# Optimization experiments

Hardware: AMD Instinct MI355X
Metric: run time of the kernel (lower is better)

The kernel has to match this reference:

```python
import jax, jax.numpy as jnp
import numpy as np

IN_CH, HID, OUT = 128, 128, 47

def _sage_conv(x_src, x_dst, src, dst, n_dst, Wl, bl, Wr):
    # mean aggregation of source features onto destination nodes
    msg_sum = jax.ops.segment_sum(x_src[src], dst, num_segments=n_dst)
    deg = jax.ops.segment_sum(jnp.ones((src.shape[0],), x_src.dtype), dst, num_segments=n_dst)
    agg = msg_sum / jnp.maximum(deg, 1.0)[:, None]
    return agg @ Wl + bl + x_dst @ Wr


def setup_inputs() -> dict:
    key = jax.random.key(0)
    ks = jax.random.split(key, 12)
    N0, N1, N2 = 200000, 100000, 20000
    E0, E1 = 1600000, 320000
    def glorot(k, fan_in, fan_out):
        s = jnp.sqrt(6.0 / (fan_in + fan_out))
        return jax.random.uniform(k, (fan_in, fan_out), jnp.float32, -s, s)
    return {
        'x': jax.random.normal(ks[0], (N0, IN_CH), jnp.float32),
        'src0': jax.random.randint(ks[1], (E0,), 0, N0),
        'dst0': jax.random.randint(ks[2], (E0,), 0, N1),
        'src1': jax.random.randint(ks[3], (E1,), 0, N1),
        'dst1': jax.random.randint(ks[4], (E1,), 0, N2),
        'n1': N1,
        'n2': N2,
        'Wl0': glorot(ks[5], IN_CH, HID),
        'bl0': jnp.zeros((HID,), jnp.float32),
        'Wr0': glorot(ks[6], IN_CH, HID),
        'Wl1': glorot(ks[7], HID, OUT),
        'bl1': jnp.zeros((OUT,), jnp.float32),
        'Wr1': glorot(ks[8], HID, OUT),
    }


def reference(x, src0, dst0, src1, dst1, n1, n2, Wl0, bl0, Wr0, Wl1, bl1, Wr1):
    # layer 0: bipartite SAGEConv + relu (dropout is identity in eval mode)
    h = _sage_conv(x, x[:n1], src0, dst0, n1, Wl0, bl0, Wr0)
    h = jax.nn.relu(h)
    # layer 1: SAGEConv to output classes
    out = _sage_conv(h, h[:n2], src1, dst1, n2, Wl1, bl1, Wr1)
    return jax.nn.log_softmax(out, axis=-1)
```

## Files before the change

### kernel.cpp

```cpp
#include <hip/hip_runtime.h>
#include <hip/hip_bf16.h>
#include <math.h>

#define N1_ROWS 100000
#define N2_ROWS 20000
#define CH 128
#define OUTC 47
#define CAP 6144
#define SCHUNK 4096

typedef __attribute__((ext_vector_type(8))) short short8;
typedef __attribute__((ext_vector_type(4))) float floatx4;

__device__ inline ushort f2b(float f) {
    union { __hip_bfloat16 b; ushort u; } cv;
    cv.b = __float2bfloat16(f);
    return cv.u;
}
__device__ inline float b2f_lo(uint u) { return __uint_as_float(u << 16); }
__device__ inline float b2f_hi(uint u) { return __uint_as_float(u & 0xffff0000u); }

__device__ inline void scatter_body(
    const int* __restrict__ src, const int* __restrict__ dst,
    uint* __restrict__ gcur, uint* __restrict__ ebuf, int E, int NB,
    int sb, uint* hist, uint* runb)
{
    const int base = sb * SCHUNK;
    const int t = threadIdx.x;

    uint d[16], s[16];
    bool ok[4];
    #pragma unroll
    for (int j = 0; j < 4; ++j) {
        int e = base + j * 1024 + t * 4;
        ok[j] = (e < E);
        if (ok[j]) {
            uint4 dv = *(const uint4*)(dst + e);
            uint4 sv = *(const uint4*)(src + e);
            d[j*4+0] = dv.x; d[j*4+1] = dv.y; d[j*4+2] = dv.z; d[j*4+3] = dv.w;
            s[j*4+0] = sv.x; s[j*4+1] = sv.y; s[j*4+2] = sv.z; s[j*4+3] = sv.w;
        }
    }

    for (int b = t; b < 512; b += 256) hist[b] = 0;
    __syncthreads();
    #pragma unroll
    for (int j = 0; j < 4; ++j)
        if (ok[j]) {
            #pragma unroll
            for (int k = 0; k < 4; ++k) atomicAdd(&hist[d[j*4+k] >> 8], 1u);
        }
    __syncthreads();
    for (int b = t; b < NB; b += 256) {
        uint c = hist[b];
        runb[b] = c ? atomicAdd(&gcur[b], c) : 0u;
        hist[b] = 0;
    }
    __syncthreads();
    #pragma unroll
    for (int j = 0; j < 4; ++j)
        if (ok[j]) {
            #pragma unroll
            for (int k = 0; k < 4; ++k) {
                uint dd = d[j*4+k];
                uint b = dd >> 8;
                uint off = runb[b] + atomicAdd(&hist[b], 1u);
                if (off < CAP)
                    ebuf[(size_t)b * CAP + off] = ((dd & 255u) << 18) | s[j*4+k];
            }
        }
}

__global__ __launch_bounds__(256) void prep(
    const float* __restrict__ x, ushort* __restrict__ xb, int n4,
    const int* __restrict__ src0, const int* __restrict__ dst0,
    uint* __restrict__ gcur0, uint* __restrict__ ebuf0, int E0, int NB0,
    const int* __restrict__ src1, const int* __restrict__ dst1,
    uint* __restrict__ gcur1, uint* __restrict__ ebuf1, int E1, int NB1,
    const float* __restrict__ Wl0, const float* __restrict__ Wr0,
    const float* __restrict__ Wl1, const float* __restrict__ Wr1,
    const float* __restrict__ bl1,
    ushort* __restrict__ W0p, ushort* __restrict__ W1p, float* __restrict__ bl1p,
    int CB, int S0, int S1)
{
    __shared__ uint hist[512];
    __shared__ uint runb[512];
    int blk = blockIdx.x;
    if (blk < S0) {
        scatter_body(src0, dst0, gcur0, ebuf0, E0, NB0, blk, hist, runb);
    } else if (blk < S0 + S1) {
        scatter_body(src1, dst1, gcur1, ebuf1, E1, NB1, blk - S0, hist, runb);
    } else if (blk == S0 + S1) {
        int t = threadIdx.x;
        for (int c = t; c < 4096; c += 256) {
            int n = c & 127; int kb = (c >> 7) & 15; int p = c >> 11;
            const float* W = p ? Wr0 : Wl0;
            __align__(16) ushort tmp[8];
            #pragma unroll
            for (int i = 0; i < 8; ++i) tmp[i] = f2b(W[(kb * 8 + i) * CH + n]);
            *(uint4*)(W0p + (size_t)c * 8) = *(const uint4*)tmp;
        }
    } else if (blk == S0 + S1 + 1) {
        int t = threadIdx.x;
        for (int c = t; c < 1536; c += 256) {
            int n = c % 48; int kb = (c / 48) & 15; int p = c / 768;
            const float* W = p ? Wr1 : Wl1;
            __align__(16) ushort tmp[8];
            #pragma unroll
            for (int i = 0; i < 8; ++i)
                tmp[i] = (n < OUTC) ? f2b(W[(kb * 8 + i) * OUTC + n]) : (ushort)0;
            *(uint4*)(W1p + (size_t)c * 8) = *(const uint4*)tmp;
        }
        if (t < 48) bl1p[t] = (t < OUTC) ? bl1[t] : -3.0e38f;
    } else {
        int i = (blk - S0 - S1 - 2) * 256 + threadIdx.x;
        if (i < n4) {
            float4 v = ((const float4*)x)[i];
            ushort4 o;
            o.x = f2b(v.x); o.y = f2b(v.y); o.z = f2b(v.z); o.w = f2b(v.w);
            ((ushort4*)xb)[i] = o;
        }
    }
}

__global__ __launch_bounds__(256) void csr_all(
    const uint* __restrict__ ebuf0, const uint* __restrict__ gcur0,
    int* __restrict__ idx0, int* __restrict__ deg0, int* __restrict__ rs0,
    int NB0, int n1,
    const uint* __restrict__ ebuf1, const uint* __restrict__ gcur1,
    int* __restrict__ idx1, int* __restrict__ deg1, int* __restrict__ rs1,
    int NB1, int n2)
{
    int b = blockIdx.x;
    const uint* ebuf; const uint* gcur;
    int* idx; int* deg; int* rs; int n;
    if (b < NB0) { ebuf = ebuf0; gcur = gcur0; idx = idx0; deg = deg0; rs = rs0; n = n1; }
    else { b -= NB0; ebuf = ebuf1; gcur = gcur1; idx = idx1; deg = deg1; rs = rs1; n = n2; }

    int t = threadIdx.x;
    __shared__ uint gsh[512];
    __shared__ uint psc[256];
    __shared__ uint hist[256];
    __shared__ uint sc[256];
    __shared__ uint lrs[256];
    __shared__ uint idxl[CAP];

    uint c0 = gcur[2 * t];     if (c0 > CAP) c0 = CAP;
    uint c1 = gcur[2 * t + 1]; if (c1 > CAP) c1 = CAP;
    uint pv = c0 + c1;
    psc[t] = pv;
    __syncthreads();
    for (int off = 1; off < 256; off <<= 1) {
        uint val = (t >= off) ? psc[t - off] : 0;
        __syncthreads();
        psc[t] += val;
        __syncthreads();
    }
    uint epair = psc[t] - pv;
    gsh[2 * t] = epair;
    gsh[2 * t + 1] = epair + c0;
    __syncthreads();

    uint cnt = gcur[b]; if (cnt > CAP) cnt = CAP;
    uint bout = gsh[b];
    size_t bin = (size_t)b * CAP;
    int row0 = b << 8;
    int nrows = n - row0; if (nrows > 256) nrows = 256;

    hist[t] = 0;
    __syncthreads();
    for (uint i0 = 0; i0 < cnt; i0 += 1024) {
        uint i = i0 + t * 4;
        uint v0 = 0, v1 = 0, v2 = 0, v3 = 0; int nv = 0;
        if (i + 3 < cnt) {
            uint4 vv = *(const uint4*)(ebuf + bin + i);
            v0 = vv.x; v1 = vv.y; v2 = vv.z; v3 = vv.w; nv = 4;
        } else if (i < cnt) {
            nv = (int)(cnt - i);
            v0 = ebuf[bin + i];
            if (nv > 1) v1 = ebuf[bin + i + 1];
            if (nv > 2) v2 = ebuf[bin + i + 2];
        }
        if (nv > 0) atomicAdd(&hist[v0 >> 18], 1u);
        if (nv > 1) atomicAdd(&hist[v1 >> 18], 1u);
        if (nv > 2) atomicAdd(&hist[v2 >> 18], 1u);
        if (nv > 3) atomicAdd(&hist[v3 >> 18], 1u);
    }
    __syncthreads();
    uint hv = hist[t];
    sc[t] = hv;
    __syncthreads();
    for (int off = 1; off < 256; off <<= 1) {
        uint val = (t >= off) ? sc[t - off] : 0;
        __syncthreads();
        sc[t] += val;
        __syncthreads();
    }
    uint lbase = sc[t] - hv;
    if (t < nrows) { deg[row0 + t] = (int)hv; rs[row0 + t] = (int)(bout + lbase); }
    lrs[t] = lbase;
    hist[t] = 0;
    __syncthreads();
    for (uint i0 = 0; i0 < cnt; i0 += 1024) {
        uint i = i0 + t * 4;
        uint v0 = 0, v1 = 0, v2 = 0, v3 = 0; int nv = 0;
        if (i + 3 < cnt) {
            uint4 vv = *(const uint4*)(ebuf + bin + i);
            v0 = vv.x; v1 = vv.y; v2 = vv.z; v3 = vv.w; nv = 4;
        } else if (i < cnt) {
            nv = (int)(cnt - i);
            v0 = ebuf[bin + i];
            if (nv > 1) v1 = ebuf[bin + i + 1];
            if (nv > 2) v2 = ebuf[bin + i + 2];
        }
        if (nv > 0) { uint r = v0 >> 18; idxl[lrs[r] + atomicAdd(&hist[r], 1u)] = v0 & 0x3FFFFu; }
        if (nv > 1) { uint r = v1 >> 18; idxl[lrs[r] + atomicAdd(&hist[r], 1u)] = v1 & 0x3FFFFu; }
        if (nv > 2) { uint r = v2 >> 18; idxl[lrs[r] + atomicAdd(&hist[r], 1u)] = v2 & 0x3FFFFu; }
        if (nv > 3) { uint r = v3 >> 18; idxl[lrs[r] + atomicAdd(&hist[r], 1u)] = v3 & 0x3FFFFu; }
    }
    __syncthreads();
    for (uint i = t; i < cnt; i += 256) idx[bout + i] = (int)idxl[i];
}

__global__ __launch_bounds__(256) void gather_mean_bb(
    const ushort* __restrict__ xb,
    const int* __restrict__ idx,
    const int* __restrict__ rs,
    const int* __restrict__ deg,
    ushort* __restrict__ aggb,
    int n)
{
    int row = blockIdx.x * 4 + (threadIdx.x >> 6);
    int lane = threadIdx.x & 63;
    if (row >= n) return;
    int start = rs[row];
    int cnt = deg[row];
    const uint* x2 = (const uint*)xb;
    float ax = 0.0f, ay = 0.0f;
    int i = 0;
    for (; i + 3 < cnt; i += 4) {
        int s0 = idx[start + i];
        int s1 = idx[start + i + 1];
        int s2 = idx[start + i + 2];
        int s3 = idx[start + i + 3];
        uint v0 = x2[(size_t)s0 * 64 + lane];
        uint v1 = x2[(size_t)s1 * 64 + lane];
        uint v2 = x2[(size_t)s2 * 64 + lane];
        uint v3 = x2[(size_t)s3 * 64 + lane];
        ax += (b2f_lo(v0) + b2f_lo(v1)) + (b2f_lo(v2) + b2f_lo(v3));
        ay += (b2f_hi(v0) + b2f_hi(v1)) + (b2f_hi(v2) + b2f_hi(v3));
    }
    for (; i < cnt; ++i) {
        uint v0 = x2[(size_t)idx[start + i] * 64 + lane];
        ax += b2f_lo(v0);
        ay += b2f_hi(v0);
    }
    float inv = 1.0f / fmaxf((float)cnt, 1.0f);
    uint o = (uint)f2b(ax * inv) | ((uint)f2b(ay * inv) << 16);
    ((uint*)aggb)[(size_t)row * 64 + lane] = o;
}

#define TM 128
__global__ __launch_bounds__(256) void gemm_mfma(
    const ushort* __restrict__ Apan,
    const ushort* __restrict__ Bpan,
    const ushort* __restrict__ Wp,
    const float* __restrict__ bias,
    ushort* __restrict__ H,
    int rows)
{
    __shared__ __align__(16) ushort As[16384];
    __shared__ __align__(16) ushort Ws[16384];

    const int tid = threadIdx.x;
    const int lane = tid & 63;
    const int wave = tid >> 6;
    const int q = lane >> 4;
    const int ln = lane & 15;
    const int rbase = blockIdx.x * TM;
    const int mrow = wave * 32;

    floatx4 acc[2][8];
    #pragma unroll
    for (int i = 0; i < 2; ++i)
        #pragma unroll
        for (int j = 0; j < 8; ++j)
            acc[i][j] = (floatx4)0.0f;

    #pragma unroll 1
    for (int phase = 0; phase < 2; ++phase) {
        const ushort* Ag = phase ? Bpan : Apan;

        {
            int m0 = tid & 15;
            int c  = tid >> 4;
            #pragma unroll
            for (int j = 0; j < 8; ++j) {
                int m = m0 + 16 * j;
                uint4 v = *(const uint4*)(Ag + (size_t)(rbase + m) * CH + c * 8);
                *(uint4*)(As + ((size_t)c * 128 + m) * 8) = v;
            }
        }
        {
            const uint4* Wg4 = (const uint4*)(Wp + phase * 16384);
            uint4* Ws4 = (uint4*)Ws;
            for (int i = tid; i < 2048; i += 256) Ws4[i] = Wg4[i];
        }
        __syncthreads();

        #pragma unroll
        for (int k = 0; k < 4; ++k) {
            int kb = k * 4 + q;
            short8 b[8];
            #pragma unroll
            for (int nt = 0; nt < 8; ++nt)
                b[nt] = *(const short8*)(Ws + ((size_t)kb * 128 + nt * 16 + ln) * 8);
            #pragma unroll
            for (int mt = 0; mt < 2; ++mt) {
                short8 a = *(const short8*)(As + ((size_t)kb * 128 + mrow + mt * 16 + ln) * 8);
                #pragma unroll
                for (int nt = 0; nt < 8; ++nt)
                    acc[mt][nt] = __builtin_amdgcn_mfma_f32_16x16x32_bf16(
                        a, b[nt], acc[mt][nt], 0, 0, 0);
            }
        }
        __syncthreads();
    }

    float bj[8];
    #pragma unroll
    for (int nt = 0; nt < 8; ++nt) bj[nt] = bias[nt * 16 + ln];

    #pragma unroll
    for (int mt = 0; mt < 2; ++mt) {
        #pragma unroll
        for (int r = 0; r < 4; ++r) {
            int grow = rbase + mrow + mt * 16 + q * 4 + r;
            if (grow < rows) {
                #pragma unroll
                for (int nt = 0; nt < 8; ++nt) {
                    float v = acc[mt][nt][r] + bj[nt];
                    v = fmaxf(v, 0.0f);
                    H[(size_t)grow * CH + nt * 16 + ln] = f2b(v);
                }
            }
        }
    }
}

__global__ __launch_bounds__(256) void gemm_mfma_l1(
    const ushort* __restrict__ Apan,
    const ushort* __restrict__ Bpan,
    const ushort* __restrict__ Wp,
    const float* __restrict__ biasp,
    float* __restrict__ out,
    int rows)
{
    __shared__ __align__(16) ushort As[16384];
    __shared__ __align__(16) ushort Ws[6144];

    const int tid = threadIdx.x;
    const int lane = tid & 63;
    const int wave = tid >> 6;
    const int q = lane >> 4;
    const int ln = lane & 15;
    const int rbase = blockIdx.x * TM;
    const int mrow = wave * 32;

    floatx4 acc[2][3];
    #pragma unroll
    for (int i = 0; i < 2; ++i)
        #pragma unroll
        for (int j = 0; j < 3; ++j)
            acc[i][j] = (floatx4)0.0f;

    #pragma unroll 1
    for (int phase = 0; phase < 2; ++phase) {
        const ushort* Ag = phase ? Bpan : Apan;
        {
            int m0 = tid & 15;
            int c  = tid >> 4;
            #pragma unroll
            for (int j = 0; j < 8; ++j) {
                int m = m0 + 16 * j;
                uint4 v = *(const uint4*)(Ag + (size_t)(rbase + m) * CH + c * 8);
                *(uint4*)(As + ((size_t)c * 128 + m) * 8) = v;
            }
        }
        {
            const uint4* Wg4 = (const uint4*)(Wp + phase * 6144);
            uint4* Ws4 = (uint4*)Ws;
            for (int i = tid; i < 768; i += 256) Ws4[i] = Wg4[i];
        }
        __syncthreads();

        #pragma unroll
        for (int k = 0; k < 4; ++k) {
            int kb = k * 4 + q;
            short8 b0 = *(const short8*)(Ws + ((size_t)kb * 48 +  0 + ln) * 8);
            short8 b1 = *(const short8*)(Ws + ((size_t)kb * 48 + 16 + ln) * 8);
            short8 b2 = *(const short8*)(Ws + ((size_t)kb * 48 + 32 + ln) * 8);
            #pragma unroll
            for (int mt = 0; mt < 2; ++mt) {
                short8 a = *(const short8*)(As + ((size_t)kb * 128 + mrow + mt * 16 + ln) * 8);
                acc[mt][0] = __builtin_amdgcn_mfma_f32_16x16x32_bf16(a, b0, acc[mt][0], 0, 0, 0);
                acc[mt][1] = __builtin_amdgcn_mfma_f32_16x16x32_bf16(a, b1, acc[mt][1], 0, 0, 0);
                acc[mt][2] = __builtin_amdgcn_mfma_f32_16x16x32_bf16(a, b2, acc[mt][2], 0, 0, 0);
            }
        }
        __syncthreads();
    }

    float b0 = biasp[ln], b1 = biasp[16 + ln], b2 = biasp[32 + ln];

    #pragma unroll
    for (int mt = 0; mt < 2; ++mt) {
        #pragma unroll
        for (int r = 0; r < 4; ++r) {
            int grow = rbase + mrow + mt * 16 + q * 4 + r;
            float v0 = acc[mt][0][r] + b0;
            float v1 = acc[mt][1][r] + b1;
            float v2 = acc[mt][2][r] + b2;
            float mx = fmaxf(v0, fmaxf(v1, v2));
            #pragma unroll
            for (int off = 1; off < 16; off <<= 1) mx = fmaxf(mx, __shfl_xor(mx, off));
            float s = expf(v0 - mx) + expf(v1 - mx) + expf(v2 - mx);
            #pragma unroll
            for (int off = 1; off < 16; off <<= 1) s += __shfl_xor(s, off);
            float ls = mx + logf(s);
            if (grow < rows) {
                out[(size_t)grow * OUTC + ln] = v0 - ls;
                out[(size_t)grow * OUTC + 16 + ln] = v1 - ls;
                if (32 + ln < OUTC) out[(size_t)grow * OUTC + 32 + ln] = v2 - ls;
            }
        }
    }
}

extern "C" void kernel_launch(void* const* d_in, const int* in_sizes, int n_in,
                              void* d_out, int out_size, void* d_ws, size_t ws_size,
                              hipStream_t stream) {
    const float* x    = (const float*)d_in[0];
    const int*   src0 = (const int*)d_in[1];
    const int*   dst0 = (const int*)d_in[2];
    const int*   src1 = (const int*)d_in[3];
    const int*   dst1 = (const int*)d_in[4];
    const float* Wl0  = (const float*)d_in[7];
    const float* bl0  = (const float*)d_in[8];
    const float* Wr0  = (const float*)d_in[9];
    const float* Wl1  = (const float*)d_in[10];
    const float* bl1  = (const float*)d_in[11];
    const float* Wr1  = (const float*)d_in[12];
    float* out = (float*)d_out;

    const int E0 = in_sizes[1];
    const int E1 = in_sizes[3];
    const int n0 = in_sizes[0] / CH;
    const int n1 = N1_ROWS, n2 = N2_ROWS;
    const int n1pad = ((n1 + TM - 1) / TM) * TM;
    const int n2pad = ((n2 + TM - 1) / TM) * TM;
    const int NB0 = (n1 + 255) >> 8;
    const int NB1 = (n2 + 255) >> 8;

    ushort* xb   = (ushort*)d_ws;
    ushort* aggb = xb + (size_t)n0 * CH;
    ushort* h    = aggb + (size_t)n1pad * CH;
    ushort* W0p  = h + (size_t)n1 * CH;
    ushort* W1p  = W0p + 32768;
    float*  bl1p = (float*)(W1p + 12288);
    int*    idx0 = (int*)(bl1p + 48);
    int*    deg0 = idx0 + E0;
    int*    rs0  = deg0 + n1;
    int*    idx1 = rs0 + n1;
    int*    deg1 = idx1 + E1;
    int*    rs1  = deg1 + n2;
    uint*   gcur0 = (uint*)(rs1 + n2);
    uint*   gcur1 = gcur0 + 512;

    uint* ebuf0 = (uint*)aggb;
    uint* ebuf1 = (uint*)h;
    ushort* agg1b = aggb;

    const int n4 = n0 * CH / 4;
    const int CB = (n4 + 255) / 256;
    const int S0 = (E0 + SCHUNK - 1) / SCHUNK;
    const int S1 = (E1 + SCHUNK - 1) / SCHUNK;

    hipMemsetAsync(gcur0, 0, 1024 * sizeof(uint), stream);
    prep<<<S0 + S1 + 2 + CB, 256, 0, stream>>>(
        x, xb, n4,
        src0, dst0, gcur0, ebuf0, E0, NB0,
        src1, dst1, gcur1, ebuf1, E1, NB1,
        Wl0, Wr0, Wl1, Wr1, bl1, W0p, W1p, bl1p,
        CB, S0, S1);
    csr_all<<<NB0 + NB1, 256, 0, stream>>>(
        ebuf0, gcur0, idx0, deg0, rs0, NB0, n1,
        ebuf1, gcur1, idx1, deg1, rs1, NB1, n2);
    gather_mean_bb<<<(n1 + 3) / 4, 256, 0, stream>>>(xb, idx0, rs0, deg0, aggb, n1);
    gemm_mfma<<<n1pad / TM, 256, 0, stream>>>(aggb, xb, W0p, bl0, h, n1);
    gather_mean_bb<<<(n2 + 3) / 4, 256, 0, stream>>>(h, idx1, rs1, deg1, agg1b, n2);
    gemm_mfma_l1<<<n2pad / TM, 256, 0, stream>>>(agg1b, h, W1p, bl1p, out, n2);
}
```

Measured before the change: 328.4 us.

## Fuse layer-0 CSR build with mean gather in one 1024-thread kernel

For layer 0, the CSR bucket sort now keeps the sorted source indices in shared memory, and the same block immediately gathers and averages the bf16 features for its 256 destination rows. This removes the global idx0/deg0/rs0 writes and reads and one kernel launch. Blocks grow to 1024 threads, and the layer-1 block offset is computed with a 512-wide scan over gcur1 only. Edge buckets move into the h buffer so aggb can be written during the fused kernel. In exchange, each block has 16 waves gathering rows and a large shared-memory footprint, which may reduce occupancy.

```diff
diff --git a/kernel.cpp b/kernel.cpp
--- a/kernel.cpp
+++ b/kernel.cpp
@@ -123,103 +123,184 @@
     }
 }
 
-__global__ __launch_bounds__(256) void csr_all(
+__global__ __launch_bounds__(1024) void csr_gather(
     const uint* __restrict__ ebuf0, const uint* __restrict__ gcur0,
-    int* __restrict__ idx0, int* __restrict__ deg0, int* __restrict__ rs0,
-    int NB0, int n1,
+    const ushort* __restrict__ xb, ushort* __restrict__ aggb, int NB0, int n1,
     const uint* __restrict__ ebuf1, const uint* __restrict__ gcur1,
     int* __restrict__ idx1, int* __restrict__ deg1, int* __restrict__ rs1,
     int NB1, int n2)
 {
-    int b = blockIdx.x;
-    const uint* ebuf; const uint* gcur;
-    int* idx; int* deg; int* rs; int n;
-    if (b < NB0) { ebuf = ebuf0; gcur = gcur0; idx = idx0; deg = deg0; rs = rs0; n = n1; }
-    else { b -= NB0; ebuf = ebuf1; gcur = gcur1; idx = idx1; deg = deg1; rs = rs1; n = n2; }
-
     int t = threadIdx.x;
-    __shared__ uint gsh[512];
-    __shared__ uint psc[256];
+    __shared__ uint idxl[CAP];
     __shared__ uint hist[256];
     __shared__ uint sc[256];
     __shared__ uint lrs[256];
-    __shared__ uint idxl[CAP];
-
-    uint c0 = gcur[2 * t];     if (c0 > CAP) c0 = CAP;
-    uint c1 = gcur[2 * t + 1]; if (c1 > CAP) c1 = CAP;
-    uint pv = c0 + c1;
-    psc[t] = pv;
-    __syncthreads();
-    for (int off = 1; off < 256; off <<= 1) {
-        uint val = (t >= off) ? psc[t - off] : 0;
-        __syncthreads();
-        psc[t] += val;
-        __syncthreads();
-    }
-    uint epair = psc[t] - pv;
-    gsh[2 * t] = epair;
-    gsh[2 * t + 1] = epair + c0;
-    __syncthreads();
-
-    uint cnt = gcur[b]; if (cnt > CAP) cnt = CAP;
-    uint bout = gsh[b];
-    size_t bin = (size_t)b * CAP;
-    int row0 = b << 8;
-    int nrows = n - row0; if (nrows > 256) nrows = 256;
-
-    hist[t] = 0;
-    __syncthreads();
-    for (uint i0 = 0; i0 < cnt; i0 += 1024) {
-        uint i = i0 + t * 4;
-        uint v0 = 0, v1 = 0, v2 = 0, v3 = 0; int nv = 0;
-        if (i + 3 < cnt) {
-            uint4 vv = *(const uint4*)(ebuf + bin + i);
-            v0 = vv.x; v1 = vv.y; v2 = vv.z; v3 = vv.w; nv = 4;
-        } else if (i < cnt) {
-            nv = (int)(cnt - i);
-            v0 = ebuf[bin + i];
-            if (nv > 1) v1 = ebuf[bin + i + 1];
-            if (nv > 2) v2 = ebuf[bin + i + 2];
-        }
-        if (nv > 0) atomicAdd(&hist[v0 >> 18], 1u);
-        if (nv > 1) atomicAdd(&hist[v1 >> 18], 1u);
-        if (nv > 2) atomicAdd(&hist[v2 >> 18], 1u);
-        if (nv > 3) atomicAdd(&hist[v3 >> 18], 1u);
-    }
-    __syncthreads();
-    uint hv = hist[t];
-    sc[t] = hv;
-    __syncthreads();
-    for (int off = 1; off < 256; off <<= 1) {
-        uint val = (t >= off) ? sc[t - off] : 0;
-        __syncthreads();
-        sc[t] += val;
-        __syncthreads();
-    }
-    uint lbase = sc[t] - hv;
-    if (t < nrows) { deg[row0 + t] = (int)hv; rs[row0 + t] = (int)(bout + lbase); }
-    lrs[t] = lbase;
-    hist[t] = 0;
-    __syncthreads();
-    for (uint i0 = 0; i0 < cnt; i0 += 1024) {
-        uint i = i0 + t * 4;
-        uint v0 = 0, v1 = 0, v2 = 0, v3 = 0; int nv = 0;
-        if (i + 3 < cnt) {
-            uint4 vv = *(const uint4*)(ebuf + bin + i);
-            v0 = vv.x; v1 = vv.y; v2 = vv.z; v3 = vv.w; nv = 4;
-        } else if (i < cnt) {
-            nv = (int)(cnt - i);
-            v0 = ebuf[bin + i];
-            if (nv > 1) v1 = ebuf[bin + i + 1];
-            if (nv > 2) v2 = ebuf[bin + i + 2];
-        }
-        if (nv > 0) { uint r = v0 >> 18; idxl[lrs[r] + atomicAdd(&hist[r], 1u)] = v0 & 0x3FFFFu; }
-        if (nv > 1) { uint r = v1 >> 18; idxl[lrs[r] + atomicAdd(&hist[r], 1u)] = v1 & 0x3FFFFu; }
-        if (nv > 2) { uint r = v2 >> 18; idxl[lrs[r] + atomicAdd(&hist[r], 1u)] = v2 & 0x3FFFFu; }
-        if (nv > 3) { uint r = v3 >> 18; idxl[lrs[r] + atomicAdd(&hist[r], 1u)] = v3 & 0x3FFFFu; }
-    }
-    __syncthreads();
-    for (uint i = t; i < cnt; i += 256) idx[bout + i] = (int)idxl[i];
+    __shared__ uint degl[256];
+    __shared__ uint psc[512];
+
+    int b = blockIdx.x;
+    if (b < NB0) {
+        uint cnt = gcur0[b]; if (cnt > CAP) cnt = CAP;
+        size_t bin = (size_t)b * CAP;
+
+        if (t < 256) hist[t] = 0;
+        __syncthreads();
+        for (uint i0 = 0; i0 < cnt; i0 += 4096) {
+            uint i = i0 + t * 4;
+            uint v0 = 0, v1 = 0, v2 = 0, v3 = 0; int nv = 0;
+            if (i + 3 < cnt) {
+                uint4 vv = *(const uint4*)(ebuf0 + bin + i);
+                v0 = vv.x; v1 = vv.y; v2 = vv.z; v3 = vv.w; nv = 4;
+            } else if (i < cnt) {
+                nv = (int)(cnt - i);
+                v0 = ebuf0[bin + i];
+                if (nv > 1) v1 = ebuf0[bin + i + 1];
+                if (nv > 2) v2 = ebuf0[bin + i + 2];
+            }
+            if (nv > 0) atomicAdd(&hist[v0 >> 18], 1u);
+            if (nv > 1) atomicAdd(&hist[v1 >> 18], 1u);
+            if (nv > 2) atomicAdd(&hist[v2 >> 18], 1u);
+            if (nv > 3) atomicAdd(&hist[v3 >> 18], 1u);
+        }
+        __syncthreads();
+        uint hv = 0;
+        if (t < 256) { hv = hist[t]; sc[t] = hv; }
+        __syncthreads();
+        for (int off = 1; off < 256; off <<= 1) {
+            uint val = 0;
+            if (t < 256 && t >= off) val = sc[t - off];
+            __syncthreads();
+            if (t < 256) sc[t] += val;
+            __syncthreads();
+        }
+        if (t < 256) { lrs[t] = sc[t] - hv; degl[t] = hv; hist[t] = 0; }
+        __syncthreads();
+        for (uint i0 = 0; i0 < cnt; i0 += 4096) {
+            uint i = i0 + t * 4;
+            uint v0 = 0, v1 = 0, v2 = 0, v3 = 0; int nv = 0;
+            if (i + 3 < cnt) {
+                uint4 vv = *(const uint4*)(ebuf0 + bin + i);
+                v0 = vv.x; v1 = vv.y; v2 = vv.z; v3 = vv.w; nv = 4;
+            } else if (i < cnt) {
+                nv = (int)(cnt - i);
+                v0 = ebuf0[bin + i];
+                if (nv > 1) v1 = ebuf0[bin + i + 1];
+                if (nv > 2) v2 = ebuf0[bin + i + 2];
+            }
+            if (nv > 0) { uint r = v0 >> 18; idxl[lrs[r] + atomicAdd(&hist[r], 1u)] = v0 & 0x3FFFFu; }
+            if (nv > 1) { uint r = v1 >> 18; idxl[lrs[r] + atomicAdd(&hist[r], 1u)] = v1 & 0x3FFFFu; }
+            if (nv > 2) { uint r = v2 >> 18; idxl[lrs[r] + atomicAdd(&hist[r], 1u)] = v2 & 0x3FFFFu; }
+            if (nv > 3) { uint r = v3 >> 18; idxl[lrs[r] + atomicAdd(&hist[r], 1u)] = v3 & 0x3FFFFu; }
+        }
+        __syncthreads();
+
+        int wave = t >> 6, lane = t & 63;
+        const uint* x2 = (const uint*)xb;
+        for (int r = wave; r < 256; r += 16) {
+            int row = (b << 8) + r;
+            if (row >= n1) break;
+            int start = (int)lrs[r];
+            int cnt_r = (int)degl[r];
+            float ax = 0.0f, ay = 0.0f;
+            int i = 0;
+            for (; i + 3 < cnt_r; i += 4) {
+                uint s0 = idxl[start + i];
+                uint s1 = idxl[start + i + 1];
+                uint s2 = idxl[start + i + 2];
+                uint s3 = idxl[start + i + 3];
+                uint v0 = x2[(size_t)s0 * 64 + lane];
+                uint v1 = x2[(size_t)s1 * 64 + lane];
+                uint v2 = x2[(size_t)s2 * 64 + lane];
+                uint v3 = x2[(size_t)s3 * 64 + lane];
+                ax += (b2f_lo(v0) + b2f_lo(v1)) + (b2f_lo(v2) + b2f_lo(v3));
+                ay += (b2f_hi(v0) + b2f_hi(v1)) + (b2f_hi(v2) + b2f_hi(v3));
+            }
+            for (; i < cnt_r; ++i) {
+                uint v0 = x2[(size_t)idxl[start + i] * 64 + lane];
+                ax += b2f_lo(v0);
+                ay += b2f_hi(v0);
+            }
+            float inv = 1.0f / fmaxf((float)cnt_r, 1.0f);
+            uint o = (uint)f2b(ax * inv) | ((uint)f2b(ay * inv) << 16);
+            ((uint*)aggb)[(size_t)row * 64 + lane] = o;
+        }
+    } else {
+        b -= NB0;
+        if (t < 512) {
+            uint c = (t < NB1) ? gcur1[t] : 0u; if (c > CAP) c = CAP;
+            psc[t] = c;
+        }
+        __syncthreads();
+        for (int off = 1; off < 512; off <<= 1) {
+            uint val = 0;
+            if (t < 512 && t >= off) val = psc[t - off];
+            __syncthreads();
+            if (t < 512) psc[t] += val;
+            __syncthreads();
+        }
+        uint cnt = gcur1[b]; if (cnt > CAP) cnt = CAP;
+        uint bout = psc[b] - cnt;
+        size_t bin = (size_t)b * CAP;
+        int row0 = b << 8;
+        int nrows = n2 - row0; if (nrows > 256) nrows = 256;
+
+        if (t < 256) hist[t] = 0;
+        __syncthreads();
+        for (uint i0 = 0; i0 < cnt; i0 += 4096) {
+            uint i = i0 + t * 4;
+            uint v0 = 0, v1 = 0, v2 = 0, v3 = 0; int nv = 0;
+            if (i + 3 < cnt) {
+                uint4 vv = *(const uint4*)(ebuf1 + bin + i);
+                v0 = vv.x; v1 = vv.y; v2 = vv.z; v3 = vv.w; nv = 4;
+            } else if (i < cnt) {
+                nv = (int)(cnt - i);
+                v0 = ebuf1[bin + i];
+                if (nv > 1) v1 = ebuf1[bin + i + 1];
+                if (nv > 2) v2 = ebuf1[bin + i + 2];
+            }
+            if (nv > 0) atomicAdd(&hist[v0 >> 18], 1u);
+            if (nv > 1) atomicAdd(&hist[v1 >> 18], 1u);
+            if (nv > 2) atomicAdd(&hist[v2 >> 18], 1u);
+            if (nv > 3) atomicAdd(&hist[v3 >> 18], 1u);
+        }
+        __syncthreads();
+        uint hv = 0;
+        if (t < 256) { hv = hist[t]; sc[t] = hv; }
+        __syncthreads();
+        for (int off = 1; off < 256; off <<= 1) {
+            uint val = 0;
+            if (t < 256 && t >= off) val = sc[t - off];
+            __syncthreads();
+            if (t < 256) sc[t] += val;
+            __syncthreads();
+        }
+        if (t < 256) {
+            uint lb = sc[t] - hv;
+            lrs[t] = lb;
+            if (t < nrows) { deg1[row0 + t] = (int)hv; rs1[row0 + t] = (int)(bout + lb); }
+            hist[t] = 0;
+        }
+        __syncthreads();
+        for (uint i0 = 0; i0 < cnt; i0 += 4096) {
+            uint i = i0 + t * 4;
+            uint v0 = 0, v1 = 0, v2 = 0, v3 = 0; int nv = 0;
+            if (i + 3 < cnt) {
+                uint4 vv = *(const uint4*)(ebuf1 + bin + i);
+                v0 = vv.x; v1 = vv.y; v2 = vv.z; v3 = vv.w; nv = 4;
+            } else if (i < cnt) {
+                nv = (int)(cnt - i);
+                v0 = ebuf1[bin + i];
+                if (nv > 1) v1 = ebuf1[bin + i + 1];
+                if (nv > 2) v2 = ebuf1[bin + i + 2];
+            }
+            if (nv > 0) { uint r = v0 >> 18; idxl[lrs[r] + atomicAdd(&hist[r], 1u)] = v0 & 0x3FFFFu; }
+            if (nv > 1) { uint r = v1 >> 18; idxl[lrs[r] + atomicAdd(&hist[r], 1u)] = v1 & 0x3FFFFu; }
+            if (nv > 2) { uint r = v2 >> 18; idxl[lrs[r] + atomicAdd(&hist[r], 1u)] = v2 & 0x3FFFFu; }
+            if (nv > 3) { uint r = v3 >> 18; idxl[lrs[r] + atomicAdd(&hist[r], 1u)] = v3 & 0x3FFFFu; }
+        }
+        __syncthreads();
+        for (uint i = t; i < cnt; i += 1024) idx1[bout + i] = (int)idxl[i];
+    }
 }
 
 __global__ __launch_bounds__(256) void gather_mean_bb(
@@ -468,17 +549,14 @@
     ushort* W0p  = h + (size_t)n1 * CH;
     ushort* W1p  = W0p + 32768;
     float*  bl1p = (float*)(W1p + 12288);
-    int*    idx0 = (int*)(bl1p + 48);
-    int*    deg0 = idx0 + E0;
-    int*    rs0  = deg0 + n1;
-    int*    idx1 = rs0 + n1;
+    int*    idx1 = (int*)(bl1p + 48);
     int*    deg1 = idx1 + E1;
     int*    rs1  = deg1 + n2;
     uint*   gcur0 = (uint*)(rs1 + n2);
     uint*   gcur1 = gcur0 + 512;
 
-    uint* ebuf0 = (uint*)aggb;
-    uint* ebuf1 = (uint*)h;
+    uint* ebuf0 = (uint*)h;
+    uint* ebuf1 = (uint*)h + (size_t)NB0 * CAP;
     ushort* agg1b = aggb;
 
     const int n4 = n0 * CH / 4;
@@ -493,10 +571,9 @@
         src1, dst1, gcur1, ebuf1, E1, NB1,
         Wl0, Wr0, Wl1, Wr1, bl1, W0p, W1p, bl1p,
         CB, S0, S1);
-    csr_all<<<NB0 + NB1, 256, 0, stream>>>(
-        ebuf0, gcur0, idx0, deg0, rs0, NB0, n1,
+    csr_gather<<<NB0 + NB1, 1024, 0, stream>>>(
+        ebuf0, gcur0, xb, aggb, NB0, n1,
         ebuf1, gcur1, idx1, deg1, rs1, NB1, n2);
-    gather_mean_bb<<<(n1 + 3) / 4, 256, 0, stream>>>(xb, idx0, rs0, deg0, aggb, n1);
     gemm_mfma<<<n1pad / TM, 256, 0, stream>>>(aggb, xb, W0p, bl0, h, n1);
     gather_mean_bb<<<(n2 + 3) / 4, 256, 0, stream>>>(h, idx1, rs1, deg1, agg1b, n2);
     gemm_mfma_l1<<<n2pad / TM, 256, 0, stream>>>(agg1b, h, W1p, bl1p, out, n2);
```

Measured after the change: 316.4 us. -3.7%, faster.
